# Optimization experiments

Measured on AMD Instinct MI355X. Metric: run time of the kernel, lower is better.

Reference implementation:

```python
import jax, jax.numpy as jnp
import numpy as np

NUM_HEADS = 4


def setup_inputs() -> dict:
    key = jax.random.key(0)
    ks = jax.random.split(key, 14)
    B, T, N, Fin, Fout, E = 4, 16, 1000, 64, 128, 12000
    s_in = 1.0 / np.sqrt(Fin)
    s_out = 1.0 / np.sqrt(Fout)
    return {
        "x": jax.random.normal(ks[0], (B, T, N, Fin), jnp.float32),
        "edge_index": jax.random.randint(ks[1], (2, E), 0, N, dtype=jnp.int64),
        # per-gate ChebConv weights (gate order: z, r, h); W0 = self term, W1 = neighbor term
        "wx0": jax.random.normal(ks[2], (3, Fin, Fout), jnp.float32) * s_in,
        "wx1": jax.random.normal(ks[3], (3, Fin, Fout), jnp.float32) * s_in,
        "bx": jax.random.normal(ks[4], (3, Fout), jnp.float32) * 0.01,
        "wh0": jax.random.normal(ks[5], (3, Fout, Fout), jnp.float32) * s_out,
        "wh1": jax.random.normal(ks[6], (3, Fout, Fout), jnp.float32) * s_out,
        "bh": jax.random.normal(ks[7], (3, Fout), jnp.float32) * 0.01,
        # torch nn.MultiheadAttention params
        "w_in": jax.random.normal(ks[8], (3 * Fout, Fout), jnp.float32) * s_out,
        "b_in": jax.random.normal(ks[9], (3 * Fout,), jnp.float32) * 0.01,
        "w_out": jax.random.normal(ks[10], (Fout, Fout), jnp.float32) * s_out,
        "b_out": jax.random.normal(ks[11], (Fout,), jnp.float32) * 0.01,
    }


def reference(x, edge_index, wx0, wx1, bx, wh0, wh1, bh, w_in, b_in, w_out, b_out):
    B, T, N, Fin = x.shape
    Fout = wx0.shape[-1]
    H = NUM_HEADS
    Dh = Fout // H
    L = B * T
    row, col = edge_index[0], edge_index[1]

    # symmetric normalization  D^{-1/2} A D^{-1/2}
    deg = jax.ops.segment_sum(jnp.ones(row.shape, x.dtype), row, num_segments=N)
    dinv = jnp.where(deg > 0, 1.0 / jnp.sqrt(jnp.maximum(deg, 1.0)), 0.0)
    normw = dinv[row] * dinv[col]  # [E]

    # [B,T,N,F] -> [N, T*B, F]  (time-major merge, matching x.view in torch)
    xg = x.transpose(2, 1, 0, 3).reshape(N, T * B, Fin)

    def conv(z, W0, W1, b):
        # ChebConv-style: self transform + sym-normalized 1-hop aggregation
        agg = jax.ops.segment_sum(normw[:, None, None] * z[col], row, num_segments=N)
        return z @ W0 + agg @ W1 + b

    # single GConvGRU step with H0 = 0
    h0 = jnp.zeros((N, T * B, Fout), x.dtype)
    Z = jax.nn.sigmoid(conv(xg, wx0[0], wx1[0], bx[0]) + conv(h0, wh0[0], wh1[0], bh[0]))
    R = jax.nn.sigmoid(conv(xg, wx0[1], wx1[1], bx[1]) + conv(h0, wh0[1], wh1[1], bh[1]))
    Ht = jnp.tanh(conv(xg, wx0[2], wx1[2], bx[2]) + conv(h0 * R, wh0[2], wh1[2], bh[2]))
    Hn = Z * h0 + (1.0 - Z) * Ht  # [N, T*B, Fout]

    # [N,T*B,F] -> [B*T, N, F]  (torch MHA layout: L=B*T, batch=N)
    a = Hn.reshape(N, T, B, Fout).transpose(2, 1, 0, 3).reshape(L, N, Fout)
    qkv = a @ w_in.T + b_in
    q, k, v = jnp.split(qkv, 3, axis=-1)

    def heads(t):
        return t.reshape(L, N, H, Dh).transpose(1, 2, 0, 3)  # [N,H,L,Dh]

    q, k, v = heads(q), heads(k), heads(v)
    att = jax.nn.softmax(jnp.einsum('nhld,nhmd->nhlm', q, k) / np.sqrt(Dh).astype(x.dtype), axis=-1)
    ctx = jnp.einsum('nhlm,nhmd->nhld', att, v).transpose(2, 0, 1, 3).reshape(L, N, Fout)
    out = ctx @ w_out.T + b_out
    return out.reshape(B, T, N, Fout)
```

## Files before the change

### kernel.cpp

```cpp
#include <hip/hip_runtime.h>
#include <math.h>

#define Nn   1000
#define FIN  64
#define FOUT 128
#define Lc   64

#define OFF_DEG    0
#define OFF_FILL   1024
#define OFF_FLAG   2048
#define OFF_ROWPTR 3072
#define OFF_CSCOL  16384
#define OFF_CSW    28672
#define OFF_WCAT   40960
#define OFF_BC     73728
#define OFF_WTIN   73984
#define OFF_WTOUT  123136
#define OFF_XGAT   147456

__global__ void k_detect(const void* edge, int* flag) {
  const long long* p = (const long long*)edge;
  int ok = 1;
  for (int i = 0; i < 16; ++i) { long long v = p[i]; if (v < 0 || v >= Nn) ok = 0; }
  *flag = ok;
}

__device__ __forceinline__ int edge_at(const void* edge, int idx, int fl) {
  return fl ? (int)((const long long*)edge)[idx] : ((const int*)edge)[idx];
}

__global__ void k_deg(const void* edge, int E, const int* flag, float* degf) {
  int e = blockIdx.x * 256 + threadIdx.x;
  if (e >= E) return;
  int r = edge_at(edge, e, *flag);
  atomicAdd(degf + r, 1.0f);
}

__global__ void k_scan(const float* degf, int* rowptr) {
  __shared__ int sc[1024];
  int tid = threadIdx.x;
  sc[tid] = (tid < Nn) ? (int)degf[tid] : 0;
  __syncthreads();
  for (int off = 1; off < 1024; off <<= 1) {
    int t = (tid >= off) ? sc[tid - off] : 0;
    __syncthreads();
    sc[tid] += t;
    __syncthreads();
  }
  if (tid == 0) rowptr[0] = 0;
  if (tid < Nn) rowptr[tid + 1] = sc[tid];
}

__global__ void k_dinv(float* degf) {
  int n = blockIdx.x * 256 + threadIdx.x;
  if (n >= Nn) return;
  float c = degf[n];
  degf[n] = (c > 0.f) ? (1.0f / sqrtf(c)) : 0.f;
}

__global__ void k_scatter(const void* edge, int E, const int* flag, const float* dinv,
                          const int* rowptr, int* fill, int* cs_col, float* cs_w) {
  int e = blockIdx.x * 256 + threadIdx.x;
  if (e >= E) return;
  int fl = *flag;
  int r = edge_at(edge, e, fl);
  int c = edge_at(edge, E + e, fl);
  int pos = rowptr[r] + atomicAdd(fill + r, 1);
  cs_col[pos] = c;
  cs_w[pos] = dinv[r] * dinv[c];
}

__global__ void k_wprep(const float* wx0, const float* wx1, const float* bx, const float* bh,
                        const float* w_in, const float* w_out, float* ws) {
  int idx = blockIdx.x * 256 + threadIdx.x;
  if (idx < 32768) {
    int f = idx >> 8, j = idx & 255;
    int g = (j < 128) ? 0 : 2, jj = j & 127;
    float v = (f < 64) ? wx0[(g * 64 + f) * 128 + jj]
                       : wx1[(g * 64 + (f - 64)) * 128 + jj];
    ws[OFF_WCAT + idx] = v;
    return;
  }
  idx -= 32768;
  if (idx < 256) {
    int g = (idx < 128) ? 0 : 2, jj = idx & 127;
    ws[OFF_BC + idx] = bx[g * 128 + jj] + bh[g * 128 + jj];
    return;
  }
  idx -= 256;
  if (idx < 49152) {
    int f = idx / 384, j = idx % 384;
    ws[OFF_WTIN + idx] = w_in[j * 128 + f];
    return;
  }
  idx -= 49152;
  if (idx < 16384) {
    int f = idx >> 7, j = idx & 127;
    ws[OFF_WTOUT + idx] = w_out[j * 128 + f];
  }
}

__global__ void k_xT(const float* __restrict__ x, float* __restrict__ xgaT) {
  int idx = blockIdx.x * 256 + threadIdx.x;
  int n = idx >> 12;
  int rem = idx & 4095;
  int f = rem >> 6, l = rem & 63;
  int b = l & 3, t = l >> 2;
  xgaT[(n << 13) + rem] = x[((b * 16 + t) * 1000 + n) * 64 + f];
}

__global__ void k_agg(float* xgaT, const int* __restrict__ rowptr,
                      const int* __restrict__ cs_col, const float* __restrict__ cs_w) {
  int n = blockIdx.x;
  int tid = threadIdx.x;
  int l4 = tid & 15, f0 = tid >> 4;
  float4 acc[4];
  #pragma unroll
  for (int i = 0; i < 4; ++i) { acc[i].x = 0.f; acc[i].y = 0.f; acc[i].z = 0.f; acc[i].w = 0.f; }
  int kb = rowptr[n], ke = rowptr[n + 1];
  for (int k = kb; k < ke; ++k) {
    int c = cs_col[k];
    float w = cs_w[k];
    #pragma unroll
    for (int i = 0; i < 4; ++i) {
      int f = f0 + 16 * i;
      float4 v = *reinterpret_cast<const float4*>(xgaT + (c * 128 + f) * 64 + l4 * 4);
      acc[i].x = fmaf(w, v.x, acc[i].x);
      acc[i].y = fmaf(w, v.y, acc[i].y);
      acc[i].z = fmaf(w, v.z, acc[i].z);
      acc[i].w = fmaf(w, v.w, acc[i].w);
    }
  }
  #pragma unroll
  for (int i = 0; i < 4; ++i) {
    int f = f0 + 16 * i;
    *reinterpret_cast<float4*>(xgaT + (n * 128 + 64 + f) * 64 + l4 * 4) = acc[i];
  }
}

__global__ __launch_bounds__(256, 1)
void k_fused(const float* __restrict__ ws, float* __restrict__ out,
             const float* __restrict__ b_in, const float* __restrict__ b_out) {
  extern __shared__ float lds[];
  float* R_XQ = lds;
  float* R_A  = lds + 8192;
  float* R_K  = lds + 16384;
  float* R_V  = lds + 24576;
  const int n = blockIdx.x;
  const int tid = threadIdx.x;

  {
    const float4* src = reinterpret_cast<const float4*>(ws + OFF_XGAT + n * 8192);
    float4* dst = reinterpret_cast<float4*>(R_XQ);
    #pragma unroll
    for (int i = 0; i < 8; ++i) dst[tid + i * 256] = src[tid + i * 256];
  }
  __syncthreads();

  {
    const int ty = tid >> 5, tx = tid & 31;
    const int r0 = ty * 8, j0 = tx * 4;
    const float* Wc = ws + OFF_WCAT;
    float accz[8][4], acch[8][4];
    {
      const float4 bz = *reinterpret_cast<const float4*>(ws + OFF_BC + j0);
      const float4 bhh = *reinterpret_cast<const float4*>(ws + OFF_BC + 128 + j0);
      const float bzv[4] = {bz.x, bz.y, bz.z, bz.w};
      const float bhv[4] = {bhh.x, bhh.y, bhh.z, bhh.w};
      #pragma unroll
      for (int r = 0; r < 8; ++r)
        #pragma unroll
        for (int c = 0; c < 4; ++c) { accz[r][c] = bzv[c]; acch[r][c] = bhv[c]; }
    }
    #pragma unroll 4
    for (int f = 0; f < 128; ++f) {
      const float4 a0 = reinterpret_cast<const float4*>(R_XQ + f * 64 + r0)[0];
      const float4 a1 = reinterpret_cast<const float4*>(R_XQ + f * 64 + r0)[1];
      const float4 wz = *reinterpret_cast<const float4*>(Wc + f * 256 + j0);
      const float4 wh = *reinterpret_cast<const float4*>(Wc + f * 256 + 128 + j0);
      const float av[8] = {a0.x, a0.y, a0.z, a0.w, a1.x, a1.y, a1.z, a1.w};
      const float wzv[4] = {wz.x, wz.y, wz.z, wz.w};
      const float whv[4] = {wh.x, wh.y, wh.z, wh.w};
      #pragma unroll
      for (int r = 0; r < 8; ++r)
        #pragma unroll
        for (int c = 0; c < 4; ++c) {
          accz[r][c] = fmaf(av[r], wzv[c], accz[r][c]);
          acch[r][c] = fmaf(av[r], whv[c], acch[r][c]);
        }
    }
    #pragma unroll
    for (int r = 0; r < 8; ++r) {
      const int l = r0 + r;
      const int lp = (l & 3) * 16 + (l >> 2);
      #pragma unroll
      for (int c = 0; c < 4; ++c) {
        const float z = 1.0f / (1.0f + __expf(-accz[r][c]));
        const float hn = (1.0f - z) * tanhf(acch[r][c]);
        R_A[(j0 + c) * 64 + lp] = hn;
      }
    }
  }
  __syncthreads();

  {
    const int ry = tid >> 5, tx = tid & 31;
    const int r0 = ry * 8;
    const int j0 = tx * 12;
    const float* wT = ws + OFF_WTIN;
    float acc[12][8];
    #pragma unroll
    for (int cc = 0; cc < 3; ++cc) {
      const float4 bv = *reinterpret_cast<const float4*>(b_in + j0 + cc * 4);
      const float bb[4] = {bv.x, bv.y, bv.z, bv.w};
      #pragma unroll
      for (int c = 0; c < 4; ++c)
        #pragma unroll
        for (int r = 0; r < 8; ++r) acc[cc * 4 + c][r] = bb[c];
    }
    #pragma unroll 2
    for (int f = 0; f < 128; ++f) {
      const float4 a0 = reinterpret_cast<const float4*>(R_A + f * 64 + r0)[0];
      const float4 a1 = reinterpret_cast<const float4*>(R_A + f * 64 + r0)[1];
      const float av[8] = {a0.x, a0.y, a0.z, a0.w, a1.x, a1.y, a1.z, a1.w};
      #pragma unroll
      for (int cc = 0; cc < 3; ++cc) {
        const float4 wv = *reinterpret_cast<const float4*>(wT + f * 384 + j0 + cc * 4);
        const float wvv[4] = {wv.x, wv.y, wv.z, wv.w};
        #pragma unroll
        for (int c = 0; c < 4; ++c)
          #pragma unroll
          for (int r = 0; r < 8; ++r)
            acc[cc * 4 + c][r] = fmaf(av[r], wvv[c], acc[cc * 4 + c][r]);
      }
    }
    #pragma unroll
    for (int cc = 0; cc < 3; ++cc) {
      const int jb = j0 + cc * 4;
      const int sec = jb >> 7;
      const int jj = jb & 127;
      if (sec == 0) {
        #pragma unroll
        for (int c = 0; c < 4; ++c)
          #pragma unroll
          for (int r = 0; r < 8; ++r)
            R_XQ[(jj + c) * 64 + r0 + r] = acc[cc * 4 + c][r];
      } else {
        float* dst = (sec == 1) ? R_K : R_V;
        #pragma unroll
        for (int r = 0; r < 8; ++r) {
          float4 v;
          v.x = acc[cc * 4 + 0][r]; v.y = acc[cc * 4 + 1][r];
          v.z = acc[cc * 4 + 2][r]; v.w = acc[cc * 4 + 3][r];
          *reinterpret_cast<float4*>(dst + (r0 + r) * 128 + jj) = v;
        }
      }
    }
  }
  __syncthreads();

  {
    const int h = tid >> 6, l = tid & 63;
    float q[32];
    #pragma unroll
    for (int d = 0; d < 32; ++d)
      q[d] = R_XQ[(h * 32 + d) * 64 + l] * 0.17677669529663687f;
    float s[64];
    #pragma unroll
    for (int m = 0; m < 64; ++m) {
      float p0 = 0.f, p1 = 0.f, p2 = 0.f, p3 = 0.f;
      const float4* kr = reinterpret_cast<const float4*>(R_K + m * 128 + h * 32);
      #pragma unroll
      for (int i = 0; i < 8; ++i) {
        const float4 kv = kr[i];
        p0 = fmaf(q[i * 4 + 0], kv.x, p0);
        p1 = fmaf(q[i * 4 + 1], kv.y, p1);
        p2 = fmaf(q[i * 4 + 2], kv.z, p2);
        p3 = fmaf(q[i * 4 + 3], kv.w, p3);
      }
      s[m] = (p0 + p1) + (p2 + p3);
    }
    float mx = s[0];
    #pragma unroll
    for (int m = 1; m < 64; ++m) mx = fmaxf(mx, s[m]);
    float s0 = 0.f, s1 = 0.f, s2 = 0.f, s3 = 0.f;
    #pragma unroll
    for (int m = 0; m < 64; m += 4) {
      s[m]     = __expf(s[m]     - mx); s0 += s[m];
      s[m + 1] = __expf(s[m + 1] - mx); s1 += s[m + 1];
      s[m + 2] = __expf(s[m + 2] - mx); s2 += s[m + 2];
      s[m + 3] = __expf(s[m + 3] - mx); s3 += s[m + 3];
    }
    const float inv = 1.0f / ((s0 + s1) + (s2 + s3));
    float c[32];
    #pragma unroll
    for (int d = 0; d < 32; ++d) c[d] = 0.f;
    #pragma unroll
    for (int m = 0; m < 64; ++m) {
      const float p = s[m];
      const float4* vr = reinterpret_cast<const float4*>(R_V + m * 128 + h * 32);
      #pragma unroll
      for (int i = 0; i < 8; ++i) {
        const float4 vv = vr[i];
        c[i * 4 + 0] = fmaf(p, vv.x, c[i * 4 + 0]);
        c[i * 4 + 1] = fmaf(p, vv.y, c[i * 4 + 1]);
        c[i * 4 + 2] = fmaf(p, vv.z, c[i * 4 + 2]);
        c[i * 4 + 3] = fmaf(p, vv.w, c[i * 4 + 3]);
      }
    }
    #pragma unroll
    for (int d = 0; d < 32; ++d)
      R_A[(h * 32 + d) * 64 + l] = c[d] * inv;
  }
  __syncthreads();

  {
    const int ry = tid >> 5, tx = tid & 31;
    const int r0 = ry * 8, j0 = tx * 4;
    const float* wT = ws + OFF_WTOUT;
    float acc[8][4];
    {
      const float4 bo = *reinterpret_cast<const float4*>(b_out + j0);
      const float bb[4] = {bo.x, bo.y, bo.z, bo.w};
      #pragma unroll
      for (int r = 0; r < 8; ++r)
        #pragma unroll
        for (int c = 0; c < 4; ++c) acc[r][c] = bb[c];
    }
    #pragma unroll 4
    for (int f = 0; f < 128; ++f) {
      const float4 a0 = reinterpret_cast<const float4*>(R_A + f * 64 + r0)[0];
      const float4 a1 = reinterpret_cast<const float4*>(R_A + f * 64 + r0)[1];
      const float4 wv = *reinterpret_cast<const float4*>(wT + f * 128 + j0);
      const float av[8] = {a0.x, a0.y, a0.z, a0.w, a1.x, a1.y, a1.z, a1.w};
      const float wvv[4] = {wv.x, wv.y, wv.z, wv.w};
      #pragma unroll
      for (int r = 0; r < 8; ++r)
        #pragma unroll
        for (int c = 0; c < 4; ++c)
          acc[r][c] = fmaf(av[r], wvv[c], acc[r][c]);
    }
    #pragma unroll
    for (int r = 0; r < 8; ++r) {
      float4 v;
      v.x = acc[r][0]; v.y = acc[r][1]; v.z = acc[r][2]; v.w = acc[r][3];
      *reinterpret_cast<float4*>(out + ((r0 + r) * 1000 + n) * 128 + j0) = v;
    }
  }
}

extern "C" void kernel_launch(void* const* d_in, const int* in_sizes, int n_in,
                              void* d_out, int out_size, void* d_ws, size_t ws_size,
                              hipStream_t stream) {
  const float* x     = (const float*)d_in[0];
  const void*  edge  = d_in[1];
  const float* wx0   = (const float*)d_in[2];
  const float* wx1   = (const float*)d_in[3];
  const float* bx    = (const float*)d_in[4];
  const float* bh    = (const float*)d_in[7];
  const float* w_in  = (const float*)d_in[8];
  const float* b_in  = (const float*)d_in[9];
  const float* w_out = (const float*)d_in[10];
  const float* b_out = (const float*)d_in[11];
  float* out = (float*)d_out;
  float* ws  = (float*)d_ws;
  int*   wsi = (int*)d_ws;
  const int E = in_sizes[1] / 2;

  (void)hipFuncSetAttribute((const void*)k_fused,
                            hipFuncAttributeMaxDynamicSharedMemorySize, 131072);

  hipMemsetAsync(d_ws, 0, 2048 * sizeof(float), stream);

  k_detect<<<1, 1, 0, stream>>>(edge, wsi + OFF_FLAG);
  k_deg<<<(E + 255) / 256, 256, 0, stream>>>(edge, E, wsi + OFF_FLAG, ws + OFF_DEG);
  k_scan<<<1, 1024, 0, stream>>>(ws + OFF_DEG, wsi + OFF_ROWPTR);
  k_dinv<<<4, 256, 0, stream>>>(ws + OFF_DEG);
  k_scatter<<<(E + 255) / 256, 256, 0, stream>>>(edge, E, wsi + OFF_FLAG, ws + OFF_DEG,
                                                 wsi + OFF_ROWPTR, wsi + OFF_FILL,
                                                 wsi + OFF_CSCOL, ws + OFF_CSW);
  k_wprep<<<385, 256, 0, stream>>>(wx0, wx1, bx, bh, w_in, w_out, ws);
  k_xT<<<16000, 256, 0, stream>>>(x, ws + OFF_XGAT);
  k_agg<<<1000, 256, 0, stream>>>(ws + OFF_XGAT, wsi + OFF_ROWPTR,
                                  wsi + OFF_CSCOL, ws + OFF_CSW);
  k_fused<<<1000, 256, 131072, stream>>>(ws, out, b_in, b_out);
}
```

Measured before the change: 460.4 us.

## Merge CSR build into one block, fuse aggregation into main kernel with 1024 threads

CSR construction (detect, degree, scan, dinv, scatter) is collapsed into a single 1024-thread block using shared-memory atomics. The weight prep and x transpose are merged into one launch, and neighbor aggregation moves into the fused kernel, so the separate agg pass and the memset are dropped. The fused kernel now runs 1024 threads per node, one lane per sequence row, with XOR-swizzled K/V in LDS. Attention uses two passes over K (max, then exp and accumulate) instead of holding scores in registers, and output stores are staged through LDS for coalescing. Fewer launches and intermediate traffic are traded for a serial single-block CSR build and recomputing QK.

```diff
diff --git a/kernel.cpp b/kernel.cpp
--- a/kernel.cpp
+++ b/kernel.cpp
@@ -1,45 +1,41 @@
 #include <hip/hip_runtime.h>
 #include <math.h>
 
-#define Nn   1000
-#define FIN  64
-#define FOUT 128
-#define Lc   64
-
-#define OFF_DEG    0
-#define OFF_FILL   1024
-#define OFF_FLAG   2048
-#define OFF_ROWPTR 3072
-#define OFF_CSCOL  16384
-#define OFF_CSW    28672
-#define OFF_WCAT   40960
-#define OFF_BC     73728
-#define OFF_WTIN   73984
-#define OFF_WTOUT  123136
-#define OFF_XGAT   147456
-
-__global__ void k_detect(const void* edge, int* flag) {
-  const long long* p = (const long long*)edge;
-  int ok = 1;
-  for (int i = 0; i < 16; ++i) { long long v = p[i]; if (v < 0 || v >= Nn) ok = 0; }
-  *flag = ok;
-}
-
-__device__ __forceinline__ int edge_at(const void* edge, int idx, int fl) {
-  return fl ? (int)((const long long*)edge)[idx] : ((const int*)edge)[idx];
-}
-
-__global__ void k_deg(const void* edge, int E, const int* flag, float* degf) {
-  int e = blockIdx.x * 256 + threadIdx.x;
-  if (e >= E) return;
-  int r = edge_at(edge, e, *flag);
-  atomicAdd(degf + r, 1.0f);
-}
-
-__global__ void k_scan(const float* degf, int* rowptr) {
+#define Nn 1000
+
+#define OFF_ROWPTR 0
+#define OFF_CSCOL  2048
+#define OFF_CSW    18432
+#define OFF_WCAT   34816
+#define OFF_BC     67584
+#define OFF_WTIN   67840
+#define OFF_WTOUT  116992
+#define OFF_XGAT   133376
+
+__global__ __launch_bounds__(1024)
+void k_csr(const void* edge, int E, int* rowptr_g, int* cs_col, float* cs_w) {
+  __shared__ int deg[1000];
+  __shared__ int rp[1001];
+  __shared__ int fill[1000];
+  __shared__ float dinv[1000];
+  __shared__ int sflag;
   __shared__ int sc[1024];
-  int tid = threadIdx.x;
-  sc[tid] = (tid < Nn) ? (int)degf[tid] : 0;
+  const int tid = threadIdx.x;
+  if (tid == 0) {
+    const long long* p = (const long long*)edge;
+    int ok = 1;
+    for (int i = 0; i < 16; ++i) { long long v = p[i]; if (v < 0 || v >= Nn) ok = 0; }
+    sflag = ok;
+  }
+  for (int i = tid; i < 1000; i += 1024) { deg[i] = 0; fill[i] = 0; }
+  __syncthreads();
+  const int fl = sflag;
+  for (int e = tid; e < E; e += 1024) {
+    int r = fl ? (int)((const long long*)edge)[e] : ((const int*)edge)[e];
+    atomicAdd(&deg[r], 1);
+  }
+  __syncthreads();
+  sc[tid] = (tid < 1000) ? deg[tid] : 0;
   __syncthreads();
   for (int off = 1; off < 1024; off <<= 1) {
     int t = (tid >= off) ? sc[tid - off] : 0;
@@ -47,32 +43,39 @@
     sc[tid] += t;
     __syncthreads();
   }
-  if (tid == 0) rowptr[0] = 0;
-  if (tid < Nn) rowptr[tid + 1] = sc[tid];
+  if (tid == 0) { rp[0] = 0; rowptr_g[0] = 0; }
+  if (tid < 1000) {
+    rp[tid + 1] = sc[tid];
+    rowptr_g[tid + 1] = sc[tid];
+    float d = (float)deg[tid];
+    dinv[tid] = (d > 0.f) ? (1.0f / sqrtf(d)) : 0.f;
+  }
+  __syncthreads();
+  for (int e = tid; e < E; e += 1024) {
+    int r = fl ? (int)((const long long*)edge)[e] : ((const int*)edge)[e];
+    int c = fl ? (int)((const long long*)edge)[E + e] : ((const int*)edge)[E + e];
+    int pos = rp[r] + atomicAdd(&fill[r], 1);
+    cs_col[pos] = c;
+    cs_w[pos] = dinv[r] * dinv[c];
+  }
 }
 
-__global__ void k_dinv(float* degf) {
-  int n = blockIdx.x * 256 + threadIdx.x;
-  if (n >= Nn) return;
-  float c = degf[n];
-  degf[n] = (c > 0.f) ? (1.0f / sqrtf(c)) : 0.f;
-}
-
-__global__ void k_scatter(const void* edge, int E, const int* flag, const float* dinv,
-                          const int* rowptr, int* fill, int* cs_col, float* cs_w) {
-  int e = blockIdx.x * 256 + threadIdx.x;
-  if (e >= E) return;
-  int fl = *flag;
-  int r = edge_at(edge, e, fl);
-  int c = edge_at(edge, E + e, fl);
-  int pos = rowptr[r] + atomicAdd(fill + r, 1);
-  cs_col[pos] = c;
-  cs_w[pos] = dinv[r] * dinv[c];
-}
-
-__global__ void k_wprep(const float* wx0, const float* wx1, const float* bx, const float* bh,
-                        const float* w_in, const float* w_out, float* ws) {
-  int idx = blockIdx.x * 256 + threadIdx.x;
+__global__ void k_prep(const float* __restrict__ x,
+                       const float* __restrict__ wx0, const float* __restrict__ wx1,
+                       const float* __restrict__ bx, const float* __restrict__ bh,
+                       const float* __restrict__ w_in, const float* __restrict__ w_out,
+                       float* __restrict__ ws) {
+  const int bid = blockIdx.x;
+  if (bid < 16000) {
+    int idx = bid * 256 + threadIdx.x;
+    int n = idx >> 12;
+    int rem = idx & 4095;
+    int f = rem >> 6, l = rem & 63;
+    int b = l & 3, t = l >> 2;
+    ws[OFF_XGAT + n * 4096 + rem] = x[((b * 16 + t) * 1000 + n) * 64 + f];
+    return;
+  }
+  int idx = (bid - 16000) * 256 + threadIdx.x;
   if (idx < 32768) {
     int f = idx >> 8, j = idx & 255;
     int g = (j < 128) ? 0 : 2, jj = j & 127;
@@ -100,252 +103,187 @@
   }
 }
 
-__global__ void k_xT(const float* __restrict__ x, float* __restrict__ xgaT) {
-  int idx = blockIdx.x * 256 + threadIdx.x;
-  int n = idx >> 12;
-  int rem = idx & 4095;
-  int f = rem >> 6, l = rem & 63;
-  int b = l & 3, t = l >> 2;
-  xgaT[(n << 13) + rem] = x[((b * 16 + t) * 1000 + n) * 64 + f];
-}
-
-__global__ void k_agg(float* xgaT, const int* __restrict__ rowptr,
-                      const int* __restrict__ cs_col, const float* __restrict__ cs_w) {
-  int n = blockIdx.x;
-  int tid = threadIdx.x;
-  int l4 = tid & 15, f0 = tid >> 4;
-  float4 acc[4];
-  #pragma unroll
-  for (int i = 0; i < 4; ++i) { acc[i].x = 0.f; acc[i].y = 0.f; acc[i].z = 0.f; acc[i].w = 0.f; }
-  int kb = rowptr[n], ke = rowptr[n + 1];
-  for (int k = kb; k < ke; ++k) {
-    int c = cs_col[k];
-    float w = cs_w[k];
-    #pragma unroll
-    for (int i = 0; i < 4; ++i) {
-      int f = f0 + 16 * i;
-      float4 v = *reinterpret_cast<const float4*>(xgaT + (c * 128 + f) * 64 + l4 * 4);
-      acc[i].x = fmaf(w, v.x, acc[i].x);
-      acc[i].y = fmaf(w, v.y, acc[i].y);
-      acc[i].z = fmaf(w, v.z, acc[i].z);
-      acc[i].w = fmaf(w, v.w, acc[i].w);
-    }
-  }
-  #pragma unroll
-  for (int i = 0; i < 4; ++i) {
-    int f = f0 + 16 * i;
-    *reinterpret_cast<float4*>(xgaT + (n * 128 + 64 + f) * 64 + l4 * 4) = acc[i];
-  }
-}
-
-__global__ __launch_bounds__(256, 1)
-void k_fused(const float* __restrict__ ws, float* __restrict__ out,
+__global__ __launch_bounds__(1024, 1)
+void k_fused(const float* __restrict__ ws, const int* __restrict__ wsi,
+             float* __restrict__ out,
              const float* __restrict__ b_in, const float* __restrict__ b_out) {
   extern __shared__ float lds[];
-  float* R_XQ = lds;
-  float* R_A  = lds + 8192;
-  float* R_K  = lds + 16384;
-  float* R_V  = lds + 24576;
+  float* R_X = lds;
+  float* R_A = lds + 8192;
+  float* R_K = lds + 16384;
+  float* R_V = lds + 24576;
   const int n = blockIdx.x;
   const int tid = threadIdx.x;
-
-  {
-    const float4* src = reinterpret_cast<const float4*>(ws + OFF_XGAT + n * 8192);
-    float4* dst = reinterpret_cast<float4*>(R_XQ);
-    #pragma unroll
-    for (int i = 0; i < 8; ++i) dst[tid + i * 256] = src[tid + i * 256];
-  }
-  __syncthreads();
-
-  {
-    const int ty = tid >> 5, tx = tid & 31;
-    const int r0 = ty * 8, j0 = tx * 4;
+  const int lane = tid & 63;
+  const int w = tid >> 6;
+
+  {
+    const int f = tid >> 4, l4 = tid & 15;
+    const float4 xv = *reinterpret_cast<const float4*>(ws + OFF_XGAT + n * 4096 + f * 64 + l4 * 4);
+    *reinterpret_cast<float4*>(R_X + f * 64 + l4 * 4) = xv;
+    const int kb = wsi[OFF_ROWPTR + n], ke = wsi[OFF_ROWPTR + n + 1];
+    float4 acc = {0.f, 0.f, 0.f, 0.f};
+    for (int k = kb; k < ke; ++k) {
+      const int c = wsi[OFF_CSCOL + k];
+      const float wgt = ws[OFF_CSW + k];
+      const float4 v = *reinterpret_cast<const float4*>(ws + OFF_XGAT + c * 4096 + f * 64 + l4 * 4);
+      acc.x = fmaf(wgt, v.x, acc.x);
+      acc.y = fmaf(wgt, v.y, acc.y);
+      acc.z = fmaf(wgt, v.z, acc.z);
+      acc.w = fmaf(wgt, v.w, acc.w);
+    }
+    *reinterpret_cast<float4*>(R_X + (64 + f) * 64 + l4 * 4) = acc;
+  }
+  __syncthreads();
+
+  {
+    float accz[8], acch[8];
+    #pragma unroll
+    for (int c = 0; c < 8; ++c) {
+      accz[c] = ws[OFF_BC + w * 8 + c];
+      acch[c] = ws[OFF_BC + 128 + w * 8 + c];
+    }
     const float* Wc = ws + OFF_WCAT;
-    float accz[8][4], acch[8][4];
-    {
-      const float4 bz = *reinterpret_cast<const float4*>(ws + OFF_BC + j0);
-      const float4 bhh = *reinterpret_cast<const float4*>(ws + OFF_BC + 128 + j0);
-      const float bzv[4] = {bz.x, bz.y, bz.z, bz.w};
-      const float bhv[4] = {bhh.x, bhh.y, bhh.z, bhh.w};
-      #pragma unroll
-      for (int r = 0; r < 8; ++r)
-        #pragma unroll
-        for (int c = 0; c < 4; ++c) { accz[r][c] = bzv[c]; acch[r][c] = bhv[c]; }
-    }
     #pragma unroll 4
     for (int f = 0; f < 128; ++f) {
-      const float4 a0 = reinterpret_cast<const float4*>(R_XQ + f * 64 + r0)[0];
-      const float4 a1 = reinterpret_cast<const float4*>(R_XQ + f * 64 + r0)[1];
-      const float4 wz = *reinterpret_cast<const float4*>(Wc + f * 256 + j0);
-      const float4 wh = *reinterpret_cast<const float4*>(Wc + f * 256 + 128 + j0);
-      const float av[8] = {a0.x, a0.y, a0.z, a0.w, a1.x, a1.y, a1.z, a1.w};
-      const float wzv[4] = {wz.x, wz.y, wz.z, wz.w};
-      const float whv[4] = {wh.x, wh.y, wh.z, wh.w};
-      #pragma unroll
-      for (int r = 0; r < 8; ++r)
-        #pragma unroll
-        for (int c = 0; c < 4; ++c) {
-          accz[r][c] = fmaf(av[r], wzv[c], accz[r][c]);
-          acch[r][c] = fmaf(av[r], whv[c], acch[r][c]);
-        }
-    }
-    #pragma unroll
-    for (int r = 0; r < 8; ++r) {
-      const int l = r0 + r;
-      const int lp = (l & 3) * 16 + (l >> 2);
-      #pragma unroll
-      for (int c = 0; c < 4; ++c) {
-        const float z = 1.0f / (1.0f + __expf(-accz[r][c]));
-        const float hn = (1.0f - z) * tanhf(acch[r][c]);
-        R_A[(j0 + c) * 64 + lp] = hn;
-      }
-    }
-  }
-  __syncthreads();
-
-  {
-    const int ry = tid >> 5, tx = tid & 31;
-    const int r0 = ry * 8;
-    const int j0 = tx * 12;
-    const float* wT = ws + OFF_WTIN;
-    float acc[12][8];
-    #pragma unroll
-    for (int cc = 0; cc < 3; ++cc) {
-      const float4 bv = *reinterpret_cast<const float4*>(b_in + j0 + cc * 4);
-      const float bb[4] = {bv.x, bv.y, bv.z, bv.w};
-      #pragma unroll
-      for (int c = 0; c < 4; ++c)
-        #pragma unroll
-        for (int r = 0; r < 8; ++r) acc[cc * 4 + c][r] = bb[c];
-    }
+      const float av = R_X[f * 64 + lane];
+      const float4 wz0 = *reinterpret_cast<const float4*>(Wc + f * 256 + w * 8);
+      const float4 wz1 = *reinterpret_cast<const float4*>(Wc + f * 256 + w * 8 + 4);
+      const float4 wh0 = *reinterpret_cast<const float4*>(Wc + f * 256 + 128 + w * 8);
+      const float4 wh1 = *reinterpret_cast<const float4*>(Wc + f * 256 + 128 + w * 8 + 4);
+      accz[0] = fmaf(av, wz0.x, accz[0]); accz[1] = fmaf(av, wz0.y, accz[1]);
+      accz[2] = fmaf(av, wz0.z, accz[2]); accz[3] = fmaf(av, wz0.w, accz[3]);
+      accz[4] = fmaf(av, wz1.x, accz[4]); accz[5] = fmaf(av, wz1.y, accz[5]);
+      accz[6] = fmaf(av, wz1.z, accz[6]); accz[7] = fmaf(av, wz1.w, accz[7]);
+      acch[0] = fmaf(av, wh0.x, acch[0]); acch[1] = fmaf(av, wh0.y, acch[1]);
+      acch[2] = fmaf(av, wh0.z, acch[2]); acch[3] = fmaf(av, wh0.w, acch[3]);
+      acch[4] = fmaf(av, wh1.x, acch[4]); acch[5] = fmaf(av, wh1.y, acch[5]);
+      acch[6] = fmaf(av, wh1.z, acch[6]); acch[7] = fmaf(av, wh1.w, acch[7]);
+    }
+    #pragma unroll
+    for (int c = 0; c < 8; ++c) {
+      const float z = 1.0f / (1.0f + __expf(-accz[c]));
+      const float hn = (1.0f - z) * tanhf(acch[c]);
+      R_A[(w * 8 + c) * 64 + lane] = hn;
+    }
+  }
+  __syncthreads();
+
+  {
+    float acc[24];
+    const int j0 = w * 24;
+    #pragma unroll
+    for (int c = 0; c < 24; ++c) acc[c] = b_in[j0 + c];
+    const float* Wt = ws + OFF_WTIN;
     #pragma unroll 2
     for (int f = 0; f < 128; ++f) {
-      const float4 a0 = reinterpret_cast<const float4*>(R_A + f * 64 + r0)[0];
-      const float4 a1 = reinterpret_cast<const float4*>(R_A + f * 64 + r0)[1];
-      const float av[8] = {a0.x, a0.y, a0.z, a0.w, a1.x, a1.y, a1.z, a1.w};
+      const float av = R_A[f * 64 + lane];
       #pragma unroll
-      for (int cc = 0; cc < 3; ++cc) {
-        const float4 wv = *reinterpret_cast<const float4*>(wT + f * 384 + j0 + cc * 4);
-        const float wvv[4] = {wv.x, wv.y, wv.z, wv.w};
-        #pragma unroll
-        for (int c = 0; c < 4; ++c)
-          #pragma unroll
-          for (int r = 0; r < 8; ++r)
-            acc[cc * 4 + c][r] = fmaf(av[r], wvv[c], acc[cc * 4 + c][r]);
+      for (int c6 = 0; c6 < 6; ++c6) {
+        const float4 wv = *reinterpret_cast<const float4*>(Wt + f * 384 + j0 + c6 * 4);
+        acc[c6 * 4 + 0] = fmaf(av, wv.x, acc[c6 * 4 + 0]);
+        acc[c6 * 4 + 1] = fmaf(av, wv.y, acc[c6 * 4 + 1]);
+        acc[c6 * 4 + 2] = fmaf(av, wv.z, acc[c6 * 4 + 2]);
+        acc[c6 * 4 + 3] = fmaf(av, wv.w, acc[c6 * 4 + 3]);
       }
     }
-    #pragma unroll
-    for (int cc = 0; cc < 3; ++cc) {
-      const int jb = j0 + cc * 4;
-      const int sec = jb >> 7;
-      const int jj = jb & 127;
-      if (sec == 0) {
-        #pragma unroll
-        for (int c = 0; c < 4; ++c)
-          #pragma unroll
-          for (int r = 0; r < 8; ++r)
-            R_XQ[(jj + c) * 64 + r0 + r] = acc[cc * 4 + c][r];
-      } else {
-        float* dst = (sec == 1) ? R_K : R_V;
-        #pragma unroll
-        for (int r = 0; r < 8; ++r) {
-          float4 v;
-          v.x = acc[cc * 4 + 0][r]; v.y = acc[cc * 4 + 1][r];
-          v.z = acc[cc * 4 + 2][r]; v.w = acc[cc * 4 + 3][r];
-          *reinterpret_cast<float4*>(dst + (r0 + r) * 128 + jj) = v;
-        }
-      }
-    }
-  }
-  __syncthreads();
-
-  {
+    const int sw = (lane & 7) << 2;
+    #pragma unroll
+    for (int c = 0; c < 24; ++c) {
+      const int j = j0 + c;
+      if (j < 128)      R_X[j * 64 + lane] = acc[c];
+      else if (j < 256) R_K[lane * 128 + ((j - 128) ^ sw)] = acc[c];
+      else              R_V[lane * 128 + ((j - 256) ^ sw)] = acc[c];
+    }
+  }
+  __syncthreads();
+
+  if (tid < 256) {
     const int h = tid >> 6, l = tid & 63;
     float q[32];
     #pragma unroll
     for (int d = 0; d < 32; ++d)
-      q[d] = R_XQ[(h * 32 + d) * 64 + l] * 0.17677669529663687f;
-    float s[64];
-    #pragma unroll
+      q[d] = R_X[(h * 32 + d) * 64 + l] * 0.17677669529663687f;
+    float mx = -1e30f;
     for (int m = 0; m < 64; ++m) {
-      float p0 = 0.f, p1 = 0.f, p2 = 0.f, p3 = 0.f;
-      const float4* kr = reinterpret_cast<const float4*>(R_K + m * 128 + h * 32);
+      const int sw = (m & 7) << 2;
+      const float* kr = R_K + m * 128;
+      float s0 = 0.f, s1 = 0.f, s2 = 0.f, s3 = 0.f;
       #pragma unroll
       for (int i = 0; i < 8; ++i) {
-        const float4 kv = kr[i];
-        p0 = fmaf(q[i * 4 + 0], kv.x, p0);
-        p1 = fmaf(q[i * 4 + 1], kv.y, p1);
-        p2 = fmaf(q[i * 4 + 2], kv.z, p2);
-        p3 = fmaf(q[i * 4 + 3], kv.w, p3);
+        const float4 kv = *reinterpret_cast<const float4*>(kr + ((h * 32 + i * 4) ^ sw));
+        s0 = fmaf(q[i * 4 + 0], kv.x, s0);
+        s1 = fmaf(q[i * 4 + 1], kv.y, s1);
+        s2 = fmaf(q[i * 4 + 2], kv.z, s2);
+        s3 = fmaf(q[i * 4 + 3], kv.w, s3);
       }
-      s[m] = (p0 + p1) + (p2 + p3);
-    }
-    float mx = s[0];
-    #pragma unroll
-    for (int m = 1; m < 64; ++m) mx = fmaxf(mx, s[m]);
-    float s0 = 0.f, s1 = 0.f, s2 = 0.f, s3 = 0.f;
-    #pragma unroll
-    for (int m = 0; m < 64; m += 4) {
-      s[m]     = __expf(s[m]     - mx); s0 += s[m];
-      s[m + 1] = __expf(s[m + 1] - mx); s1 += s[m + 1];
-      s[m + 2] = __expf(s[m + 2] - mx); s2 += s[m + 2];
-      s[m + 3] = __expf(s[m + 3] - mx); s3 += s[m + 3];
-    }
-    const float inv = 1.0f / ((s0 + s1) + (s2 + s3));
-    float c[32];
-    #pragma unroll
-    for (int d = 0; d < 32; ++d) c[d] = 0.f;
-    #pragma unroll
+      mx = fmaxf(mx, (s0 + s1) + (s2 + s3));
+    }
+    float den = 0.f;
+    float cx[32];
+    #pragma unroll
+    for (int d = 0; d < 32; ++d) cx[d] = 0.f;
     for (int m = 0; m < 64; ++m) {
-      const float p = s[m];
-      const float4* vr = reinterpret_cast<const float4*>(R_V + m * 128 + h * 32);
+      const int sw = (m & 7) << 2;
+      const float* kr = R_K + m * 128;
+      float s0 = 0.f, s1 = 0.f, s2 = 0.f, s3 = 0.f;
       #pragma unroll
       for (int i = 0; i < 8; ++i) {
-        const float4 vv = vr[i];
-        c[i * 4 + 0] = fmaf(p, vv.x, c[i * 4 + 0]);
-        c[i * 4 + 1] = fmaf(p, vv.y, c[i * 4 + 1]);
-        c[i * 4 + 2] = fmaf(p, vv.z, c[i * 4 + 2]);
-        c[i * 4 + 3] = fmaf(p, vv.w, c[i * 4 + 3]);
+        const float4 kv = *reinterpret_cast<const float4*>(kr + ((h * 32 + i * 4) ^ sw));
+        s0 = fmaf(q[i * 4 + 0], kv.x, s0);
+        s1 = fmaf(q[i * 4 + 1], kv.y, s1);
+        s2 = fmaf(q[i * 4 + 2], kv.z, s2);
+        s3 = fmaf(q[i * 4 + 3], kv.w, s3);
       }
-    }
+      const float p = __expf(((s0 + s1) + (s2 + s3)) - mx);
+      den += p;
+      const float* vr = R_V + m * 128;
+      #pragma unroll
+      for (int i = 0; i < 8; ++i) {
+        const float4 vv = *reinterpret_cast<const float4*>(vr + ((h * 32 + i * 4) ^ sw));
+        cx[i * 4 + 0] = fmaf(p, vv.x, cx[i * 4 + 0]);
+        cx[i * 4 + 1] = fmaf(p, vv.y, cx[i * 4 + 1]);
+        cx[i * 4 + 2] = fmaf(p, vv.z, cx[i * 4 + 2]);
+        cx[i * 4 + 3] = fmaf(p, vv.w, cx[i * 4 + 3]);
+      }
+    }
+    const float inv = 1.0f / den;
     #pragma unroll
     for (int d = 0; d < 32; ++d)
-      R_A[(h * 32 + d) * 64 + l] = c[d] * inv;
-  }
-  __syncthreads();
-
-  {
-    const int ry = tid >> 5, tx = tid & 31;
-    const int r0 = ry * 8, j0 = tx * 4;
-    const float* wT = ws + OFF_WTOUT;
-    float acc[8][4];
-    {
-      const float4 bo = *reinterpret_cast<const float4*>(b_out + j0);
-      const float bb[4] = {bo.x, bo.y, bo.z, bo.w};
-      #pragma unroll
-      for (int r = 0; r < 8; ++r)
-        #pragma unroll
-        for (int c = 0; c < 4; ++c) acc[r][c] = bb[c];
-    }
+      R_A[(h * 32 + d) * 64 + l] = cx[d] * inv;
+  }
+  __syncthreads();
+
+  {
+    float acc[8];
+    #pragma unroll
+    for (int c = 0; c < 8; ++c) acc[c] = b_out[w * 8 + c];
+    const float* Wt = ws + OFF_WTOUT;
     #pragma unroll 4
     for (int f = 0; f < 128; ++f) {
-      const float4 a0 = reinterpret_cast<const float4*>(R_A + f * 64 + r0)[0];
-      const float4 a1 = reinterpret_cast<const float4*>(R_A + f * 64 + r0)[1];
-      const float4 wv = *reinterpret_cast<const float4*>(wT + f * 128 + j0);
-      const float av[8] = {a0.x, a0.y, a0.z, a0.w, a1.x, a1.y, a1.z, a1.w};
-      const float wvv[4] = {wv.x, wv.y, wv.z, wv.w};
-      #pragma unroll
-      for (int r = 0; r < 8; ++r)
-        #pragma unroll
-        for (int c = 0; c < 4; ++c)
-          acc[r][c] = fmaf(av[r], wvv[c], acc[r][c]);
-    }
-    #pragma unroll
-    for (int r = 0; r < 8; ++r) {
-      float4 v;
-      v.x = acc[r][0]; v.y = acc[r][1]; v.z = acc[r][2]; v.w = acc[r][3];
-      *reinterpret_cast<float4*>(out + ((r0 + r) * 1000 + n) * 128 + j0) = v;
-    }
+      const float av = R_A[f * 64 + lane];
+      const float4 w0 = *reinterpret_cast<const float4*>(Wt + f * 128 + w * 8);
+      const float4 w1 = *reinterpret_cast<const float4*>(Wt + f * 128 + w * 8 + 4);
+      acc[0] = fmaf(av, w0.x, acc[0]); acc[1] = fmaf(av, w0.y, acc[1]);
+      acc[2] = fmaf(av, w0.z, acc[2]); acc[3] = fmaf(av, w0.w, acc[3]);
+      acc[4] = fmaf(av, w1.x, acc[4]); acc[5] = fmaf(av, w1.y, acc[5]);
+      acc[6] = fmaf(av, w1.z, acc[6]); acc[7] = fmaf(av, w1.w, acc[7]);
+    }
+    float4 o0 = {acc[0], acc[1], acc[2], acc[3]};
+    float4 o1 = {acc[4], acc[5], acc[6], acc[7]};
+    *reinterpret_cast<float4*>(R_K + lane * 132 + w * 8) = o0;
+    *reinterpret_cast<float4*>(R_K + lane * 132 + w * 8 + 4) = o1;
+  }
+  __syncthreads();
+
+  {
+    const int l = tid >> 4, j8 = tid & 15;
+    const int lpp = (l & 3) * 16 + (l >> 2);
+    const float4 a = *reinterpret_cast<const float4*>(R_K + l * 132 + j8 * 8);
+    const float4 b = *reinterpret_cast<const float4*>(R_K + l * 132 + j8 * 8 + 4);
+    float* dst = out + ((size_t)(lpp * 1000 + n)) * 128 + j8 * 8;
+    *reinterpret_cast<float4*>(dst) = a;
+    *reinterpret_cast<float4*>(dst + 4) = b;
   }
 }
 
@@ -370,18 +308,8 @@
   (void)hipFuncSetAttribute((const void*)k_fused,
                             hipFuncAttributeMaxDynamicSharedMemorySize, 131072);
 
-  hipMemsetAsync(d_ws, 0, 2048 * sizeof(float), stream);
-
-  k_detect<<<1, 1, 0, stream>>>(edge, wsi + OFF_FLAG);
-  k_deg<<<(E + 255) / 256, 256, 0, stream>>>(edge, E, wsi + OFF_FLAG, ws + OFF_DEG);
-  k_scan<<<1, 1024, 0, stream>>>(ws + OFF_DEG, wsi + OFF_ROWPTR);
-  k_dinv<<<4, 256, 0, stream>>>(ws + OFF_DEG);
-  k_scatter<<<(E + 255) / 256, 256, 0, stream>>>(edge, E, wsi + OFF_FLAG, ws + OFF_DEG,
-                                                 wsi + OFF_ROWPTR, wsi + OFF_FILL,
-                                                 wsi + OFF_CSCOL, ws + OFF_CSW);
-  k_wprep<<<385, 256, 0, stream>>>(wx0, wx1, bx, bh, w_in, w_out, ws);
-  k_xT<<<16000, 256, 0, stream>>>(x, ws + OFF_XGAT);
-  k_agg<<<1000, 256, 0, stream>>>(ws + OFF_XGAT, wsi + OFF_ROWPTR,
-                                  wsi + OFF_CSCOL, ws + OFF_CSW);
-  k_fused<<<1000, 256, 131072, stream>>>(ws, out, b_in, b_out);
+  k_csr<<<1, 1024, 0, stream>>>(edge, E, wsi + OFF_ROWPTR,
+                                wsi + OFF_CSCOL, ws + OFF_CSW);
+  k_prep<<<16385, 256, 0, stream>>>(x, wx0, wx1, bx, bh, w_in, w_out, ws);
+  k_fused<<<1000, 1024, 131072, stream>>>(ws, wsi, out, b_in, b_out);
 }
```

After: 979.3 us. 113% more time.
